# Optimization experiments

Hardware: AMD Instinct MI355X
Metric: run time of the kernel (lower is better)

The kernel has to match this reference:

```python
import jax, jax.numpy as jnp
import numpy as np

K = 10
EPS = 1e-5  # BatchNorm eps, eval mode with running_mean=0, running_var=1


def mish(x):
    return x * jnp.tanh(jax.nn.softplus(x))


def knn_idx(x, k):
    # x: (B, C, N); returns (B, N, k) indices of k nearest neighbors (incl. self)
    xx = jnp.sum(x * x, axis=1)                      # (B, N)
    inner = jnp.einsum('bcn,bcm->bnm', x, x)         # (B, N, N)
    neg_d = 2.0 * inner - xx[:, :, None] - xx[:, None, :]
    return jax.lax.top_k(neg_d, k)[1]


def graph_feature(x, k):
    # x: (B, C, N) -> edge features (B, 2C, N, k): cat(nbr - x, x)
    idx = knn_idx(x, k)
    x_t = jnp.transpose(x, (0, 2, 1))                # (B, N, C)
    nbr = jax.vmap(lambda xt, ix: xt[ix])(x_t, idx)  # (B, N, k, C)
    ctr = jnp.broadcast_to(x_t[:, :, None, :], nbr.shape)
    edge = jnp.concatenate([nbr - ctr, ctr], axis=-1)
    return jnp.transpose(edge, (0, 3, 1, 2))


def block2d(x, W, g, b):
    # Conv2d(kernel=1, bias=False) + BatchNorm2d(eval) + Mish
    y = jnp.einsum('oi,bink->bonk', W, x)
    y = y * (g / jnp.sqrt(1.0 + EPS))[None, :, None, None] + b[None, :, None, None]
    return mish(y)


def block1d(x, W, g, b):
    # Conv1d(kernel=1, bias=False) + BatchNorm1d(eval) + Mish
    y = jnp.einsum('oi,bin->bon', W, x)
    y = y * (g / jnp.sqrt(1.0 + EPS))[None, :, None] + b[None, :, None]
    return mish(y)


def setup_inputs() -> dict:
    key = jax.random.key(0)
    ks = jax.random.split(key, 32)
    B, N = 8, 4096
    x = jax.random.normal(ks[0], (B, 3, N), dtype=jnp.float32)

    def w(k, o, i):
        return jax.random.normal(k, (o, i), dtype=jnp.float32) * np.float32(np.sqrt(2.0 / i))

    W1 = w(ks[1], 64, 6)
    W2 = w(ks[2], 64, 128)
    W3 = w(ks[3], 128, 128)
    W4 = w(ks[4], 128, 128)
    W5 = w(ks[5], 128, 256)
    W6 = w(ks[6], 64, 128)
    W7 = w(ks[7], 64, 128)
    W8 = w(ks[8], 64, 128)
    W9 = w(ks[9], 2, 64)

    bn_sizes = [64, 64, 128, 128, 128, 64, 64, 64]
    gs, bs = [], []
    for i, c in enumerate(bn_sizes):
        gs.append(1.0 + 0.1 * jax.random.normal(ks[10 + i], (c,), dtype=jnp.float32))
        bs.append(0.1 * jax.random.normal(ks[20 + i], (c,), dtype=jnp.float32))

    d = {'x': x, 'W1': W1, 'W2': W2, 'W3': W3, 'W4': W4, 'W5': W5,
         'W6': W6, 'W7': W7, 'W8': W8, 'W9': W9}
    for i in range(8):
        d['g%d' % (i + 1)] = gs[i]
        d['b%d' % (i + 1)] = bs[i]
    return d


def reference(x, W1, W2, W3, W4, W5, W6, W7, W8, W9,
              g1, g2, g3, g4, g5, g6, g7, g8,
              b1, b2, b3, b4, b5, b6, b7, b8):
    e = graph_feature(x, K)                      # (B, 6, N, k)
    x1 = jnp.max(block2d(e, W1, g1, b1), axis=-1)  # (B, 64, N)
    e = graph_feature(x1, K)                     # (B, 128, N, k)
    x2 = jnp.max(block2d(e, W2, g2, b2), axis=-1)  # (B, 64, N)
    e = graph_feature(x2, K)                     # (B, 128, N, k)
    x3 = jnp.max(block2d(e, W3, g3, b3), axis=-1)  # (B, 128, N)
    h = block1d(x3, W4, g4, b4)                  # (B, 128, N)
    h = block1d(jnp.concatenate([h, x3], axis=1), W5, g5, b5)  # (B, 128, N)
    h = block1d(h, W6, g6, b6)                   # (B, 64, N)
    h = block1d(jnp.concatenate([h, x2], axis=1), W7, g7, b7)  # (B, 64, N)
    h = block1d(jnp.concatenate([h, x1], axis=1), W8, g8, b8)  # (B, 64, N)
    return jnp.einsum('oi,bin->bon', W9, h)      # (B, 2, N)
```

## Files before the change

kernel.cpp:

```cpp
#include <hip/hip_runtime.h>
#include <hip/hip_bf16.h>
#include <math.h>
#include <float.h>

#define B_ 8
#define N_ 4096
#define M_ (B_*N_)
#define KNN 10

typedef unsigned long long ull;
typedef __attribute__((ext_vector_type(8))) short s16x8;
typedef __attribute__((ext_vector_type(4))) float f32x4;

__device__ __forceinline__ float mishf(float x){
  float sp = (x > 20.f) ? x : __logf(1.f + __expf(x));
  float e2 = __expf(-2.f*sp);
  float th = (1.f - e2) / (1.f + e2);
  return x * th;
}

__device__ __forceinline__ ull shfl_xor_u64(ull v, int mask){
  unsigned lo = (unsigned)v, hi = (unsigned)(v >> 32);
  lo = (unsigned)__shfl_xor((int)lo, mask);
  hi = (unsigned)__shfl_xor((int)hi, mask);
  return ((ull)hi << 32) | lo;
}
__device__ __forceinline__ ull shfl_u64(ull v, int src){
  unsigned lo = (unsigned)v, hi = (unsigned)(v >> 32);
  lo = (unsigned)__shfl((int)lo, src);
  hi = (unsigned)__shfl((int)hi, src);
  return ((ull)hi << 32) | lo;
}
__device__ __forceinline__ int mbcnt_lt(ull mask){
  return __builtin_amdgcn_mbcnt_hi((unsigned)(mask>>32),
         __builtin_amdgcn_mbcnt_lo((unsigned)mask, 0));
}
__device__ __forceinline__ unsigned mono_u32(float f){
  unsigned u = __float_as_uint(f);
  return u ^ ((unsigned)((int)u >> 31) | 0x80000000u);
}
__device__ __forceinline__ float unmono(unsigned vk){
  unsigned u = (vk & 0x80000000u) ? (vk ^ 0x80000000u) : ~vk;
  return __uint_as_float(u);
}
__device__ __forceinline__ void gload_lds16(const void* g, void* l){
  __builtin_amdgcn_global_load_lds(
      (const __attribute__((address_space(1))) unsigned int*)g,
      (__attribute__((address_space(3))) unsigned int*)l, 16, 0, 0);
}

__global__ __launch_bounds__(256) void k_transpose_x(const float* __restrict__ x,
                                                     float* __restrict__ xp,
                                                     float4* __restrict__ xp4){
  int n = blockIdx.x*256 + threadIdx.x;
  if (n >= M_) return;
  int b = n >> 12, i = n & (N_-1);
  const float* xb = x + (size_t)b*3*N_;
  float v0 = xb[i], v1 = xb[N_+i], v2 = xb[2*N_+i];
  float* o = xp + (size_t)n*3;
  o[0]=v0; o[1]=v1; o[2]=v2;
  float s = fmaf(v0,v0,0.f); s = fmaf(v1,v1,s); s = fmaf(v2,v2,s);
  xp4[n] = make_float4(v0, v1, v2, -0.5f*s);
}

template<int C>
__global__ __launch_bounds__(256) void k_xx(const float* __restrict__ X,
                                            float* __restrict__ xx){
  int n = blockIdx.x*256 + threadIdx.x;
  if (n >= M_) return;
  const float* r = X + (size_t)n*C;
  float s = 0.f;
#pragma unroll
  for (int c=0;c<C;c++){ float v=r[c]; s = fmaf(v,v,s); }
  xx[n] = s;
}

__global__ __launch_bounds__(256) void k_cvt(const float* __restrict__ X,
                                             ushort* __restrict__ Xhi,
                                             ushort* __restrict__ Xlo){
  int i = blockIdx.x*256 + threadIdx.x;
  const float4* src = (const float4*)X + (size_t)i*2;
  float4 v0 = src[0], v1 = src[1];
  float vv[8] = {v0.x,v0.y,v0.z,v0.w,v1.x,v1.y,v1.z,v1.w};
  ushort h[8], l[8];
#pragma unroll
  for (int e=0;e<8;e++){
    __hip_bfloat16 hb = __float2bfloat16(vv[e]);
    float hf = __bfloat162float(hb);
    __hip_bfloat16 lb = __float2bfloat16(vv[e]-hf);
    h[e] = *(ushort*)&hb; l[e] = *(ushort*)&lb;
  }
  uint4 hp, lp;
  hp.x = (unsigned)h[0] | ((unsigned)h[1]<<16);
  hp.y = (unsigned)h[2] | ((unsigned)h[3]<<16);
  hp.z = (unsigned)h[4] | ((unsigned)h[5]<<16);
  hp.w = (unsigned)h[6] | ((unsigned)h[7]<<16);
  lp.x = (unsigned)l[0] | ((unsigned)l[1]<<16);
  lp.y = (unsigned)l[2] | ((unsigned)l[3]<<16);
  lp.z = (unsigned)l[4] | ((unsigned)l[5]<<16);
  lp.w = (unsigned)l[6] | ((unsigned)l[7]<<16);
  *(uint4*)(Xhi + (size_t)i*8) = hp;
  *(uint4*)(Xlo + (size_t)i*8) = lp;
}

__global__ __launch_bounds__(256) void k_knn3s(const float4* __restrict__ xp4,
                                               ull* __restrict__ part){
  const int bid   = blockIdx.x;
  const int piece = bid & 7;
  const int rg    = (bid >> 3) & 15;
  const int b     = bid >> 7;
  const int t     = threadIdx.x;
  const int row   = rg*256 + t;
  const float4 xi = xp4[(size_t)b*N_ + row];
  const float4* xj = xp4 + (size_t)b*N_ + piece*512;
  const int jbase = piece*512;

  ull kq[KNN];
#pragma unroll
  for (int q=0;q<KNN;q++) kq[q] = 0x007FFFFF00000000ull;
  float T = -INFINITY;

  for (int jc=0; jc<512; jc+=8){
    float4 c[8];
#pragma unroll
    for (int u=0;u<8;u++) c[u] = xj[jc+u];
#pragma unroll
    for (int u=0;u<8;u++){
      float a = fmaf(xi.x, c[u].x, 0.f);
      a = fmaf(xi.y, c[u].y, a);
      a = fmaf(xi.z, c[u].z, a);
      float v = a + c[u].w;
      if (v > T){
        unsigned jinv = 4095u - (unsigned)(jbase + jc + u);
        ull ck = ((ull)mono_u32(v)<<32) | jinv;
#pragma unroll
        for (int q=0;q<KNN;q++){
          ull hi = ck > kq[q] ? ck : kq[q];
          ull lo = ck > kq[q] ? kq[q] : ck;
          kq[q] = hi; ck = lo;
        }
        T = unmono((unsigned)(kq[KNN-1] >> 32));
      }
    }
  }

  ull* o = part + ((size_t)(b*N_ + row)*8 + piece)*KNN;
#pragma unroll
  for (int q=0;q<KNN;q++) o[q] = kq[q];
}

__global__ __launch_bounds__(256) void k_knnmerge8(const ull* __restrict__ part,
                                                   int* __restrict__ idxout){
  int row = blockIdx.x*256 + threadIdx.x;
  if (row >= M_) return;
  const ull* p = part + (size_t)row*8*KNN;
  unsigned P = 0;
  int* o = idxout + (size_t)row*KNN;
  for (int s=0;s<KNN;s++){
    ull best = 0; int bl = 0;
#pragma unroll
    for (int l=0;l<8;l++){
      unsigned pl = (P >> (4*l)) & 15u;
      ull k = p[l*KNN + pl];
      if (k > best){ best = k; bl = l; }
    }
    P += 1u << (4*bl);
    o[s] = (int)(4095u - ((unsigned)best & 4095u));
  }
}

__global__ __launch_bounds__(256,2) void k_knn64m(const ushort* __restrict__ Xhi,
                                                  const ushort* __restrict__ Xlo,
                                                  const float* __restrict__ xx,
                                                  int* __restrict__ idxout){
  constexpr int JT  = 128;
  constexpr int NT  = N_/JT;
  constexpr int CAP = 320;
  __shared__ ushort XJhi[2][JT*64];
  __shared__ ushort XJlo[2][JT*64];
  __shared__ float  halfxx[2][JT];
  __shared__ ull    buf[4][CAP];

  const int t    = threadIdx.x;
  const int w    = t >> 6;
  const int lane = t & 63;
  const int b    = blockIdx.x & 7;
  const int i0   = (blockIdx.x >> 3) * 64;
  const size_t rowbase = (size_t)b*N_;
  const float* xxb = xx + rowbase;

  const int arow = i0 + w*16 + (lane & 15);
  const ushort* Ah = Xhi + (rowbase + arow)*64;
  const ushort* Al = Xlo + (rowbase + arow)*64;
  const int ko = (lane >> 4)*8;
  s16x8 aH0 = *(const s16x8*)(Ah + ko);
  s16x8 aH1 = *(const s16x8*)(Ah + 32 + ko);
  s16x8 aL0 = *(const s16x8*)(Al + ko);
  s16x8 aL1 = *(const s16x8*)(Al + 32 + ko);

  ull kq[KNN];
#pragma unroll
  for (int q=0;q<KNN;q++) kq[q]=0ull;
  float Treg = -INFINITY;

  const int lr = lane >> 3;
  const int sc = (lane & 7) ^ lr;

  {
#pragma unroll
    for (int seg=0; seg<4; ++seg){
      const int row0 = w*32 + seg*8;
      gload_lds16(Xhi + (rowbase + row0 + lr)*64 + sc*8, &XJhi[0][row0*64]);
      gload_lds16(Xlo + (rowbase + row0 + lr)*64 + sc*8, &XJlo[0][row0*64]);
    }
    if (t < JT) halfxx[0][t] = 0.5f*xxb[t];
  }
  __syncthreads();

  for (int jt = 0; jt < NT; ++jt){
    const int cur = jt & 1;
    const int j0 = jt*JT;

    float hnext = 0.f;
    if (jt < NT-1){
      const size_t nb0 = rowbase + j0 + JT;
#pragma unroll
      for (int seg=0; seg<4; ++seg){
        const int row0 = w*32 + seg*8;
        gload_lds16(Xhi + (nb0 + row0 + lr)*64 + sc*8, &XJhi[cur^1][row0*64]);
        gload_lds16(Xlo + (nb0 + row0 + lr)*64 + sc*8, &XJlo[cur^1][row0*64]);
      }
      if (t < JT) hnext = 0.5f*xxb[j0 + JT + t];
    }

    f32x4 acc[8];
#pragma unroll
    for (int cb=0;cb<8;cb++) acc[cb] = (f32x4){0.f,0.f,0.f,0.f};

#pragma unroll
    for (int cb=0;cb<8;cb++){
      const int brow = cb*16 + (lane & 15);
      const unsigned sw = ((unsigned)(brow & 7)) << 4;
      const char* ph = (const char*)&XJhi[cur][0] + brow*128;
      const char* pl = (const char*)&XJlo[cur][0] + brow*128;
      const int kb0 = (int)((unsigned)((lane>>4)<<4) ^ sw);
      const int kb1 = (int)((unsigned)(64 | ((lane>>4)<<4)) ^ sw);
      s16x8 bh0 = *(const s16x8*)(ph + kb0);
      s16x8 bl0 = *(const s16x8*)(pl + kb0);
      s16x8 bh1 = *(const s16x8*)(ph + kb1);
      s16x8 bl1 = *(const s16x8*)(pl + kb1);
      f32x4 a = acc[cb];
      a = __builtin_amdgcn_mfma_f32_16x16x32_bf16(aH0, bh0, a, 0,0,0);
      a = __builtin_amdgcn_mfma_f32_16x16x32_bf16(aH0, bl0, a, 0,0,0);
      a = __builtin_amdgcn_mfma_f32_16x16x32_bf16(aL0, bh0, a, 0,0,0);
      a = __builtin_amdgcn_mfma_f32_16x16x32_bf16(aL0, bl0, a, 0,0,0);
      a = __builtin_amdgcn_mfma_f32_16x16x32_bf16(aH1, bh1, a, 0,0,0);
      a = __builtin_amdgcn_mfma_f32_16x16x32_bf16(aH1, bl1, a, 0,0,0);
      a = __builtin_amdgcn_mfma_f32_16x16x32_bf16(aL1, bh1, a, 0,0,0);
      a = __builtin_amdgcn_mfma_f32_16x16x32_bf16(aL1, bl1, a, 0,0,0);
      acc[cb] = a;
    }

    float hx[8];
#pragma unroll
    for (int cb=0;cb<8;cb++) hx[cb] = halfxx[cur][cb*16 + (lane & 15)];

    if (jt < NT-1 && t < JT) halfxx[cur^1][t] = hnext;

    if (jt == 0){
#pragma unroll
      for (int reg=0;reg<4;reg++){
        const unsigned rl = (unsigned)((lane>>4)*4 + reg);
        ull k8[8];
#pragma unroll
        for (int cb=0;cb<8;cb++){
          float v = acc[cb][reg] - hx[cb];
          unsigned jinv = 4095u - (unsigned)(cb*16 + (lane & 15));
          k8[cb] = ((ull)mono_u32(v)<<32) | ((ull)jinv<<4) | rl;
        }
#pragma unroll
        for (int q=0;q<KNN;q++){
          ull m = k8[0];
#pragma unroll
          for (int s=1;s<8;s++) m = m > k8[s] ? m : k8[s];
          ull v1 = shfl_xor_u64(m,1); m = m>v1?m:v1;
          ull v2 = shfl_xor_u64(m,2); m = m>v2?m:v2;
          ull v4 = shfl_xor_u64(m,4); m = m>v4?m:v4;
          ull v8 = shfl_xor_u64(m,8); m = m>v8?m:v8;
          ull mv = shfl_u64(m, (lane>>2)<<4);
          if (lane < 16 && (lane&3)==reg) kq[q] = mv;
#pragma unroll
          for (int s=0;s<8;s++) k8[s] = (k8[s]==m) ? 0ull : k8[s];
        }
      }
      Treg = unmono((unsigned)(kq[KNN-1] >> 32));
    } else {
      float Tf[4];
#pragma unroll
      for (int reg=0;reg<4;reg++) Tf[reg] = __shfl(Treg, (lane>>4)*4 + reg);
      int cnt = 0;
#pragma unroll
      for (int cb=0;cb<8;cb++){
#pragma unroll
        for (int reg=0;reg<4;reg++){
          float v = acc[cb][reg] - hx[cb];
          bool pass = v >= Tf[reg];
          ull mask = __ballot(pass);
          if (mask){
            if (pass){
              int slot = cnt + mbcnt_lt(mask);
              unsigned jinv = 4095u - (unsigned)(j0 + cb*16 + (lane & 15));
              ull key = ((ull)mono_u32(v)<<32) | ((ull)jinv<<4)
                        | (unsigned)((lane>>4)*4 + reg);
              if (slot < CAP) buf[w][slot] = key;
            }
            cnt += __popcll(mask);
          }
        }
      }
      if (cnt){
        int nb = cnt < CAP ? cnt : CAP;
        int pad = (4 - (nb & 3)) & 3;
        if (lane < pad && nb + lane < CAP) buf[w][nb + lane] = 0ull;
        int nb4 = nb + pad; if (nb4 > CAP) nb4 = CAP;
        for (int e=0;e<nb4;e+=4){
          ull c0=buf[w][e+0], c1=buf[w][e+1], c2=buf[w][e+2], c3=buf[w][e+3];
#pragma unroll
          for (int u=0;u<4;u++){
            ull k64 = (u==0)?c0:(u==1)?c1:(u==2)?c2:c3;
            if ((int)(k64 & 15ull) == lane && k64 > kq[KNN-1]){
              ull ck = k64;
#pragma unroll
              for (int q=0;q<KNN;q++){
                ull hi = ck > kq[q] ? ck : kq[q];
                ull lo = ck > kq[q] ? kq[q] : ck;
                kq[q] = hi; ck = lo;
              }
            }
          }
        }
        Treg = unmono((unsigned)(kq[KNN-1] >> 32));
      }
    }
    __syncthreads();
  }

  if (lane < 16){
    int* o = idxout + ((size_t)b*N_ + i0 + w*16 + lane)*KNN;
#pragma unroll
    for (int q=0;q<KNN;q++) o[q] = (int)(4095u - (unsigned)((kq[q]>>4) & 4095ull));
  }
}

template<int PT>
__global__ __launch_bounds__(256) void k_gemm(
    const float* __restrict__ X1, int C1,
    const float* __restrict__ X2, int C2,
    const float* __restrict__ W, int hmask, int hshift, int wstride, int hoff,
    const float* __restrict__ g, const float* __restrict__ bb, int act,
    float* __restrict__ Y, int Pfull)
{
  constexpr int CPT = PT/16;
  constexpr int WLS = PT + 4;
  __shared__ float Xt[32*68];
  __shared__ float Wt[32*WLS];
  const int t  = threadIdx.x;
  const int r0 = blockIdx.x*64;
  const int p0 = blockIdx.y*PT;
  const int cg = t & 15, rg = t >> 4;
  const int C = C1 + C2;
  const int nkt = (C + 31) >> 5;

  float acc[4][CPT];
#pragma unroll
  for (int a=0;a<4;a++)
#pragma unroll
    for (int c=0;c<CPT;c++) acc[a][c]=0.f;

  for (int kt = 0; kt < nkt; ++kt){
    const int k0 = kt*32;
#pragma unroll
    for (int e = t; e < 64*32; e += 256){
      int kk = e & 31, r = e >> 5;
      int gk = k0 + kk;
      float v = 0.f;
      if (gk < C1) v = X1[(size_t)(r0+r)*C1 + gk];
      else if (gk < C) v = X2[(size_t)(r0+r)*C2 + (gk - C1)];
      Xt[kk*68 + r] = v;
    }
#pragma unroll
    for (int e = t; e < PT*32; e += 256){
      int kk = e & 31, p = e >> 5;
      int gp = p0 + p;
      int wrow = (gp & hmask)*wstride + (gp >> hshift)*hoff;
      int gk = k0 + kk;
      Wt[kk*WLS + p] = (gk < C) ? W[(size_t)wrow + gk] : 0.f;
    }
    __syncthreads();
#pragma unroll
    for (int kk=0;kk<32;kk++){
      float4 xv = *(const float4*)&Xt[kk*68 + rg*4];
      float xr[4] = {xv.x, xv.y, xv.z, xv.w};
      float wv[CPT];
#pragma unroll
      for (int c4=0;c4<CPT/4;c4++){
        float4 w4 = *(const float4*)&Wt[kk*WLS + cg*CPT + c4*4];
        wv[c4*4+0]=w4.x; wv[c4*4+1]=w4.y; wv[c4*4+2]=w4.z; wv[c4*4+3]=w4.w;
      }
#pragma unroll
      for (int rr=0;rr<4;rr++)
#pragma unroll
        for (int cc=0;cc<CPT;cc++)
          acc[rr][cc] = fmaf(xr[rr], wv[cc], acc[rr][cc]);
    }
    __syncthreads();
  }

  const float srs = rsqrtf(1.f + 1e-5f);
  float sv[CPT], bvv[CPT];
#pragma unroll
  for (int cc=0;cc<CPT;cc++){
    int gp = p0 + cg*CPT + cc;
    if (g){ sv[cc] = g[gp]*srs; bvv[cc] = bb[gp]; } else { sv[cc]=1.f; bvv[cc]=0.f; }
  }
#pragma unroll
  for (int rr=0;rr<4;rr++){
    size_t row = r0 + rg*4 + rr;
    float* yr = Y + row*(size_t)Pfull + p0 + cg*CPT;
#pragma unroll
    for (int c4=0;c4<CPT/4;c4++){
      float y0 = sv[c4*4+0]*acc[rr][c4*4+0] + bvv[c4*4+0];
      float y1 = sv[c4*4+1]*acc[rr][c4*4+1] + bvv[c4*4+1];
      float y2 = sv[c4*4+2]*acc[rr][c4*4+2] + bvv[c4*4+2];
      float y3 = sv[c4*4+3]*acc[rr][c4*4+3] + bvv[c4*4+3];
      if (act){ y0=mishf(y0); y1=mishf(y1); y2=mishf(y2); y3=mishf(y3); }
      *(float4*)&yr[c4*4] = make_float4(y0,y1,y2,y3);
    }
  }
}

template<int O>
__global__ __launch_bounds__(256) void k_edgemax(
    const float* __restrict__ ua, const int* __restrict__ idx,
    const float* __restrict__ g, const float* __restrict__ bb,
    float* __restrict__ Y)
{
  constexpr int TPR = O/4;
  const int gt = blockIdx.x*256 + threadIdx.x;
  const int m  = gt / TPR;
  const int og = gt % TPR;
  if (m >= M_) return;
  const int base = m & ~(N_-1);
  const int P = 2*O;
  const float4 u0 = *(const float4*)&ua[(size_t)m*P + og*4];
  const float4 a0 = *(const float4*)&ua[(size_t)m*P + O + og*4];
  const float srs = rsqrtf(1.f + 1e-5f);
  const float4 gv  = *(const float4*)&g[og*4];
  const float4 bv4 = *(const float4*)&bb[og*4];
  const float sx = gv.x*srs, sy = gv.y*srs, sz = gv.z*srs, sw = gv.w*srs;
  const float cx = a0.x - u0.x, cy = a0.y - u0.y, cz = a0.z - u0.z, cw = a0.w - u0.w;
  float mx = -INFINITY, my = -INFINITY, mz = -INFINITY, mw = -INFINITY;
  const int* id = idx + (size_t)m*KNN;
#pragma unroll
  for (int k=0;k<KNN;k++){
    int j = id[k];
    const float4 uj = *(const float4*)&ua[(size_t)(base + j)*P + og*4];
    float zx = fmaf(sx, uj.x + cx, bv4.x);
    float zy = fmaf(sy, uj.y + cy, bv4.y);
    float zz = fmaf(sz, uj.z + cz, bv4.z);
    float zw = fmaf(sw, uj.w + cw, bv4.w);
    mx = fmaxf(mx, mishf(zx));
    my = fmaxf(my, mishf(zy));
    mz = fmaxf(mz, mishf(zz));
    mw = fmaxf(mw, mishf(zw));
  }
  *(float4*)&Y[(size_t)m*O + og*4] = make_float4(mx,my,mz,mw);
}

__global__ __launch_bounds__(256) void k_final(const float* __restrict__ h,
                                               const float* __restrict__ W9,
                                               float* __restrict__ out){
  __shared__ float w[128];
  const int t = threadIdx.x;
  if (t < 128) w[t] = W9[t];
  __syncthreads();
  const int m = blockIdx.x*256 + t;
  if (m >= M_) return;
  const int b = m >> 12, i = m & (N_-1);
  const float* hr = h + (size_t)m*64;
  float s0 = 0.f, s1 = 0.f;
#pragma unroll
  for (int c=0;c<64;c++){ float v = hr[c]; s0 = fmaf(w[c], v, s0); s1 = fmaf(w[64+c], v, s1); }
  out[((size_t)b*2 + 0)*N_ + i] = s0;
  out[((size_t)b*2 + 1)*N_ + i] = s1;
}

extern "C" void kernel_launch(void* const* d_in, const int* in_sizes, int n_in,
                              void* d_out, int out_size, void* d_ws, size_t ws_size,
                              hipStream_t stream)
{
  const float* x  = (const float*)d_in[0];
  const float* W1 = (const float*)d_in[1];
  const float* W2 = (const float*)d_in[2];
  const float* W3 = (const float*)d_in[3];
  const float* W4 = (const float*)d_in[4];
  const float* W5 = (const float*)d_in[5];
  const float* W6 = (const float*)d_in[6];
  const float* W7 = (const float*)d_in[7];
  const float* W8 = (const float*)d_in[8];
  const float* W9 = (const float*)d_in[9];
  const float* g1 = (const float*)d_in[10]; const float* b1 = (const float*)d_in[11];
  const float* g2 = (const float*)d_in[12]; const float* b2 = (const float*)d_in[13];
  const float* g3 = (const float*)d_in[14]; const float* b3 = (const float*)d_in[15];
  const float* g4 = (const float*)d_in[16]; const float* b4 = (const float*)d_in[17];
  const float* g5 = (const float*)d_in[18]; const float* b5 = (const float*)d_in[19];
  const float* g6 = (const float*)d_in[20]; const float* b6 = (const float*)d_in[21];
  const float* g7 = (const float*)d_in[22]; const float* b7 = (const float*)d_in[23];
  const float* g8 = (const float*)d_in[24]; const float* b8 = (const float*)d_in[25];
  float* out = (float*)d_out;

  float* ws  = (float*)d_ws;
  float* xp  = ws;
  float* xx  = xp + 98304;
  float4* xp4 = (float4*)(xx + 32768);
  int*   idx = (int*)(xx + 32768 + 131072);
  float* ua  = (float*)(idx + 327680);
  float* x1  = ua + 8388608;
  float* x2  = x1 + 2097152;
  float* x3  = x2 + 2097152;
  float* h4  = x3 + 4194304;
  float* h5  = h4 + 4194304;
  float* h6  = x3;
  float* h7  = h4;
  float* h8  = h5;
  ushort* Xhi = (ushort*)ua;
  ushort* Xlo = (ushort*)(ua + 1048576);
  ull*    part = (ull*)(ua + 2097152);

  const dim3 blk(256);
  const float* nullf = nullptr;

  k_transpose_x<<<dim3(M_/256), blk, 0, stream>>>(x, xp, xp4);
  k_knn3s<<<dim3(1024), blk, 0, stream>>>(xp4, part);
  k_knnmerge8<<<dim3(M_/256), blk, 0, stream>>>(part, idx);
  k_gemm<128><<<dim3(M_/64, 1), blk, 0, stream>>>(xp, 3, nullf, 0,
      W1, 63, 6, 6, 3, nullf, nullf, 0, ua, 128);
  k_edgemax<64><<<dim3(M_*16/256), blk, 0, stream>>>(ua, idx, g1, b1, x1);

  k_xx<64><<<dim3(M_/256), blk, 0, stream>>>(x1, xx);
  k_cvt<<<dim3(M_*64/(8*256)), blk, 0, stream>>>(x1, Xhi, Xlo);
  k_knn64m<<<dim3(512), blk, 0, stream>>>(Xhi, Xlo, xx, idx);
  k_gemm<128><<<dim3(M_/64, 1), blk, 0, stream>>>(x1, 64, nullf, 0,
      W2, 63, 6, 128, 64, nullf, nullf, 0, ua, 128);
  k_edgemax<64><<<dim3(M_*16/256), blk, 0, stream>>>(ua, idx, g2, b2, x2);

  k_xx<64><<<dim3(M_/256), blk, 0, stream>>>(x2, xx);
  k_cvt<<<dim3(M_*64/(8*256)), blk, 0, stream>>>(x2, Xhi, Xlo);
  k_knn64m<<<dim3(512), blk, 0, stream>>>(Xhi, Xlo, xx, idx);
  k_gemm<128><<<dim3(M_/64, 2), blk, 0, stream>>>(x2, 64, nullf, 0,
      W3, 127, 7, 128, 64, nullf, nullf, 0, ua, 256);
  k_edgemax<128><<<dim3(M_*32/256), blk, 0, stream>>>(ua, idx, g3, b3, x3);

  k_gemm<128><<<dim3(M_/64, 1), blk, 0, stream>>>(x3, 128, nullf, 0,
      W4, 127, 7, 128, 0, g4, b4, 1, h4, 128);
  k_gemm<128><<<dim3(M_/64, 1), blk, 0, stream>>>(h4, 128, x3, 128,
      W5, 127, 7, 256, 0, g5, b5, 1, h5, 128);
  k_gemm<64><<<dim3(M_/64, 1), blk, 0, stream>>>(h5, 128, nullf, 0,
      W6, 63, 6, 128, 0, g6, b6, 1, h6, 64);
  k_gemm<64><<<dim3(M_/64, 1), blk, 0, stream>>>(h6, 64, x2, 64,
      W7, 63, 6, 128, 0, g7, b7, 1, h7, 64);
  k_gemm<64><<<dim3(M_/64, 1), blk, 0, stream>>>(h7, 64, x1, 64,
      W8, 63, 6, 128, 0, g8, b8, 1, h8, 64);
  k_final<<<dim3(M_/256), blk, 0, stream>>>(h8, W9, out);
}
```

Baseline: 1.447 ms.

## Split 64-dim KNN over two candidate halves and merge partial top-k lists

The 64-channel KNN kernel now splits the candidate range into two halves of 2048 points per query tile. This doubles the grid from 512 to 1024 blocks, and each block writes its sorted top-10 keys to a partial buffer that a new merge kernel combines. The candidate tile shrinks from 128 to 64, the overflow buffer shrinks, and launch bounds rise to 4 waves per SIMD for more occupancy. The cost is an extra kernel launch and partial-buffer traffic, plus a second threshold warm-up per half. The pass comparison changes from >= to >, which filters ties more aggressively.

After: 1.768 ms. +22.2%, slower.

```diff
diff --git a/kernel.cpp b/kernel.cpp
--- a/kernel.cpp
+++ b/kernel.cpp
@@ -169,13 +169,32 @@
   }
 }
 
-__global__ __launch_bounds__(256,2) void k_knn64m(const ushort* __restrict__ Xhi,
+__global__ __launch_bounds__(256) void k_knnmerge2(const ull* __restrict__ part,
+                                                   int* __restrict__ idxout){
+  int row = blockIdx.x*256 + threadIdx.x;
+  if (row >= M_) return;
+  const ull* pa = part + (size_t)row*2*KNN;
+  const ull* pb = pa + KNN;
+  int ia=0, ib=0;
+  int* o = idxout + (size_t)row*KNN;
+#pragma unroll
+  for (int s=0;s<KNN;s++){
+    ull ka = (ia < KNN) ? pa[ia] : 0ull;
+    ull kb = (ib < KNN) ? pb[ib] : 0ull;
+    bool ta = ka > kb;
+    ull k = ta ? ka : kb;
+    o[s] = (int)(4095u - (unsigned)((k>>4) & 4095ull));
+    ia += ta ? 1 : 0; ib += ta ? 0 : 1;
+  }
+}
+
+__global__ __launch_bounds__(256,4) void k_knn64m(const ushort* __restrict__ Xhi,
                                                   const ushort* __restrict__ Xlo,
                                                   const float* __restrict__ xx,
-                                                  int* __restrict__ idxout){
-  constexpr int JT  = 128;
-  constexpr int NT  = N_/JT;
-  constexpr int CAP = 320;
+                                                  ull* __restrict__ part){
+  constexpr int JT  = 64;
+  constexpr int NT  = 2048/JT;
+  constexpr int CAP = 224;
   __shared__ ushort XJhi[2][JT*64];
   __shared__ ushort XJlo[2][JT*64];
   __shared__ float  halfxx[2][JT];
@@ -184,8 +203,12 @@
   const int t    = threadIdx.x;
   const int w    = t >> 6;
   const int lane = t & 63;
-  const int b    = blockIdx.x & 7;
-  const int i0   = (blockIdx.x >> 3) * 64;
+  const int bid  = blockIdx.x;
+  const int b    = bid & 7;
+  const int rest = bid >> 3;
+  const int i0   = (rest >> 1) * 64;
+  const int half = rest & 1;
+  const int jbase = half * 2048;
   const size_t rowbase = (size_t)b*N_;
   const float* xxb = xx + rowbase;
 
@@ -208,37 +231,37 @@
 
   {
 #pragma unroll
-    for (int seg=0; seg<4; ++seg){
-      const int row0 = w*32 + seg*8;
-      gload_lds16(Xhi + (rowbase + row0 + lr)*64 + sc*8, &XJhi[0][row0*64]);
-      gload_lds16(Xlo + (rowbase + row0 + lr)*64 + sc*8, &XJlo[0][row0*64]);
-    }
-    if (t < JT) halfxx[0][t] = 0.5f*xxb[t];
+    for (int seg=0; seg<2; ++seg){
+      const int row0 = w*16 + seg*8;
+      gload_lds16(Xhi + (rowbase + jbase + row0 + lr)*64 + sc*8, &XJhi[0][row0*64]);
+      gload_lds16(Xlo + (rowbase + jbase + row0 + lr)*64 + sc*8, &XJlo[0][row0*64]);
+    }
+    if (t < JT) halfxx[0][t] = 0.5f*xxb[jbase + t];
   }
   __syncthreads();
 
   for (int jt = 0; jt < NT; ++jt){
     const int cur = jt & 1;
-    const int j0 = jt*JT;
+    const int j0 = jbase + jt*JT;
 
     float hnext = 0.f;
     if (jt < NT-1){
       const size_t nb0 = rowbase + j0 + JT;
 #pragma unroll
-      for (int seg=0; seg<4; ++seg){
-        const int row0 = w*32 + seg*8;
+      for (int seg=0; seg<2; ++seg){
+        const int row0 = w*16 + seg*8;
         gload_lds16(Xhi + (nb0 + row0 + lr)*64 + sc*8, &XJhi[cur^1][row0*64]);
         gload_lds16(Xlo + (nb0 + row0 + lr)*64 + sc*8, &XJlo[cur^1][row0*64]);
       }
       if (t < JT) hnext = 0.5f*xxb[j0 + JT + t];
     }
 
-    f32x4 acc[8];
-#pragma unroll
-    for (int cb=0;cb<8;cb++) acc[cb] = (f32x4){0.f,0.f,0.f,0.f};
-
-#pragma unroll
-    for (int cb=0;cb<8;cb++){
+    f32x4 acc[4];
+#pragma unroll
+    for (int cb=0;cb<4;cb++) acc[cb] = (f32x4){0.f,0.f,0.f,0.f};
+
+#pragma unroll
+    for (int cb=0;cb<4;cb++){
       const int brow = cb*16 + (lane & 15);
       const unsigned sw = ((unsigned)(brow & 7)) << 4;
       const char* ph = (const char*)&XJhi[cur][0] + brow*128;
@@ -261,9 +284,9 @@
       acc[cb] = a;
     }
 
-    float hx[8];
-#pragma unroll
-    for (int cb=0;cb<8;cb++) hx[cb] = halfxx[cur][cb*16 + (lane & 15)];
+    float hx[4];
+#pragma unroll
+    for (int cb=0;cb<4;cb++) hx[cb] = halfxx[cur][cb*16 + (lane & 15)];
 
     if (jt < NT-1 && t < JT) halfxx[cur^1][t] = hnext;
 
@@ -271,18 +294,18 @@
 #pragma unroll
       for (int reg=0;reg<4;reg++){
         const unsigned rl = (unsigned)((lane>>4)*4 + reg);
-        ull k8[8];
-#pragma unroll
-        for (int cb=0;cb<8;cb++){
+        ull k4[4];
+#pragma unroll
+        for (int cb=0;cb<4;cb++){
           float v = acc[cb][reg] - hx[cb];
-          unsigned jinv = 4095u - (unsigned)(cb*16 + (lane & 15));
-          k8[cb] = ((ull)mono_u32(v)<<32) | ((ull)jinv<<4) | rl;
+          unsigned jinv = 4095u - (unsigned)(j0 + cb*16 + (lane & 15));
+          k4[cb] = ((ull)mono_u32(v)<<32) | ((ull)jinv<<4) | rl;
         }
 #pragma unroll
         for (int q=0;q<KNN;q++){
-          ull m = k8[0];
-#pragma unroll
-          for (int s=1;s<8;s++) m = m > k8[s] ? m : k8[s];
+          ull m = k4[0];
+#pragma unroll
+          for (int s=1;s<4;s++) m = m > k4[s] ? m : k4[s];
           ull v1 = shfl_xor_u64(m,1); m = m>v1?m:v1;
           ull v2 = shfl_xor_u64(m,2); m = m>v2?m:v2;
           ull v4 = shfl_xor_u64(m,4); m = m>v4?m:v4;
@@ -290,7 +313,7 @@
           ull mv = shfl_u64(m, (lane>>2)<<4);
           if (lane < 16 && (lane&3)==reg) kq[q] = mv;
 #pragma unroll
-          for (int s=0;s<8;s++) k8[s] = (k8[s]==m) ? 0ull : k8[s];
+          for (int s=0;s<4;s++) k4[s] = (k4[s]==m) ? 0ull : k4[s];
         }
       }
       Treg = unmono((unsigned)(kq[KNN-1] >> 32));
@@ -300,11 +323,11 @@
       for (int reg=0;reg<4;reg++) Tf[reg] = __shfl(Treg, (lane>>4)*4 + reg);
       int cnt = 0;
 #pragma unroll
-      for (int cb=0;cb<8;cb++){
+      for (int cb=0;cb<4;cb++){
 #pragma unroll
         for (int reg=0;reg<4;reg++){
           float v = acc[cb][reg] - hx[cb];
-          bool pass = v >= Tf[reg];
+          bool pass = v > Tf[reg];
           ull mask = __ballot(pass);
           if (mask){
             if (pass){
@@ -346,9 +369,9 @@
   }
 
   if (lane < 16){
-    int* o = idxout + ((size_t)b*N_ + i0 + w*16 + lane)*KNN;
-#pragma unroll
-    for (int q=0;q<KNN;q++) o[q] = (int)(4095u - (unsigned)((kq[q]>>4) & 4095ull));
+    ull* o = part + ((size_t)((b*N_ + i0 + w*16 + lane)*2 + half))*KNN;
+#pragma unroll
+    for (int q=0;q<KNN;q++) o[q] = kq[q];
   }
 }
 
@@ -549,14 +572,16 @@
 
   k_xx<64><<<dim3(M_/256), blk, 0, stream>>>(x1, xx);
   k_cvt<<<dim3(M_*64/(8*256)), blk, 0, stream>>>(x1, Xhi, Xlo);
-  k_knn64m<<<dim3(512), blk, 0, stream>>>(Xhi, Xlo, xx, idx);
+  k_knn64m<<<dim3(1024), blk, 0, stream>>>(Xhi, Xlo, xx, part);
+  k_knnmerge2<<<dim3(M_/256), blk, 0, stream>>>(part, idx);
   k_gemm<128><<<dim3(M_/64, 1), blk, 0, stream>>>(x1, 64, nullf, 0,
       W2, 63, 6, 128, 64, nullf, nullf, 0, ua, 128);
   k_edgemax<64><<<dim3(M_*16/256), blk, 0, stream>>>(ua, idx, g2, b2, x2);
 
   k_xx<64><<<dim3(M_/256), blk, 0, stream>>>(x2, xx);
   k_cvt<<<dim3(M_*64/(8*256)), blk, 0, stream>>>(x2, Xhi, Xlo);
-  k_knn64m<<<dim3(512), blk, 0, stream>>>(Xhi, Xlo, xx, idx);
+  k_knn64m<<<dim3(1024), blk, 0, stream>>>(Xhi, Xlo, xx, part);
+  k_knnmerge2<<<dim3(M_/256), blk, 0, stream>>>(part, idx);
   k_gemm<128><<<dim3(M_/64, 2), blk, 0, stream>>>(x2, 64, nullf, 0,
       W3, 127, 7, 128, 64, nullf, nullf, 0, ua, 256);
   k_edgemax<128><<<dim3(M_*32/256), blk, 0, stream>>>(ua, idx, g3, b3, x3);
```
